# Optimization experiments

Measured on AMD Instinct MI355X. Metric: run time of the kernel, lower is better.

Reference implementation:

```python
import jax, jax.numpy as jnp
import numpy as np

R = 2  # decimation factor


def _cheby1_sos(N=8, rp=0.05, Wn=1.0 / R):
    """Chebyshev type-I lowpass, second-order sections (matches scipy.signal.cheby1 math)."""
    eps = np.sqrt(10.0 ** (rp / 10.0) - 1.0)
    mu = np.arcsinh(1.0 / eps) / N
    k = np.arange(1, N + 1)
    theta = np.pi * (2 * k - 1) / (2 * N)
    # analog prototype poles (no zeros)
    p = -np.sinh(mu) * np.sin(theta) + 1j * np.cosh(mu) * np.cos(theta)
    gain = np.real(np.prod(-p))
    if N % 2 == 0:
        gain /= np.sqrt(1.0 + eps * eps)
    # prewarp + lp2lp
    fs = 2.0
    warped = 2.0 * fs * np.tan(np.pi * Wn / fs)
    p = p * warped
    gain = gain * warped ** N
    # bilinear transform (zeros -> z=-1, order N)
    fs2 = 2.0 * fs
    pz = (fs2 + p) / (fs2 - p)
    gain = gain / np.real(np.prod(fs2 - p))
    # pair complex-conjugate poles into biquads (N even, all complex)
    pp = pz[np.imag(pz) > 0]
    a1 = -2.0 * np.real(pp)
    a2 = np.abs(pp) ** 2
    g = gain ** (1.0 / len(pp))  # distribute gain evenly across sections
    b0 = np.full(len(pp), g)
    sos = np.stack([b0, 2.0 * b0, b0, np.ones(len(pp)), a1, a2], axis=1)
    return sos  # [nsec, 6] float64


_SOS = _cheby1_sos()


def _sosfilt(x):
    """Cascaded biquads, direct form II transposed, zero initial state. x: [B, T]."""
    B = x.shape[0]
    nsec = _SOS.shape[0]
    b0 = jnp.asarray(_SOS[:, 0], x.dtype)
    b1 = jnp.asarray(_SOS[:, 1], x.dtype)
    b2 = jnp.asarray(_SOS[:, 2], x.dtype)
    a1 = jnp.asarray(_SOS[:, 4], x.dtype)
    a2 = jnp.asarray(_SOS[:, 5], x.dtype)

    def step(carry, xt):  # carry: (z1, z2) each [B, nsec]; xt: [B]
        z1, z2 = carry
        y = xt
        nz1, nz2 = [], []
        for s in range(nsec):  # fixed small unroll over sections
            out = b0[s] * y + z1[:, s]
            nz1.append(b1[s] * y + z2[:, s] - a1[s] * out)
            nz2.append(b2[s] * y - a2[s] * out)
            y = out
        return (jnp.stack(nz1, axis=1), jnp.stack(nz2, axis=1)), y

    z0 = jnp.zeros((B, nsec), x.dtype)
    _, ys = jax.lax.scan(step, (z0, z0), x.T)  # scan over time
    return ys.T  # [B, T]


def setup_inputs() -> dict:
    key = jax.random.key(0)
    x = jax.random.normal(key, (32, 131072), dtype=jnp.float32)
    return {"x": x}


def reference(x) -> jnp.ndarray:
    y = _sosfilt(x)
    return y[..., ::R]
```

## Files before the change

### kernel.cpp

```cpp
#include <hip/hip_runtime.h>
#include <cmath>
#include <complex>


#define T_LEN   131072
#define B_ROWS  32
#define L_CHUNK 64
#define H_WARM  192
#define CPR     (T_LEN / L_CHUNK)
#define NTHREADS (B_ROWS * CPR)

struct Coef { float g; float a1[4]; float a2[4]; };

__device__ __forceinline__ float4 ldg4(const float* __restrict__ p, int idx) {
    if (idx >= 0) return *reinterpret_cast<const float4*>(p + idx);
    return make_float4(0.f, 0.f, 0.f, 0.f);
}

__global__ __launch_bounds__(256) void cheby_decimate_kernel(
    const float* __restrict__ x, float* __restrict__ out, Coef c)
{
    const int tid   = blockIdx.x * blockDim.x + threadIdx.x;
    const int row   = tid >> 11;
    const int chunk = tid & (CPR - 1);
    const float* __restrict__ xr = x + (size_t)row * T_LEN;
    float* __restrict__ orow = out + (size_t)row * (T_LEN / 2)
                                   + (size_t)chunk * (L_CHUNK / 2);

    const float g    = c.g;
    const float na10 = -c.a1[0], na20 = -c.a2[0];
    const float na11 = -c.a1[1], na21 = -c.a2[1];
    const float na12 = -c.a1[2], na22 = -c.a2[2];
    const float na13 = -c.a1[3], na23 = -c.a2[3];

    float z11=0.f,z12=0.f, z21=0.f,z22=0.f, z31=0.f,z32=0.f, z41=0.f,z42=0.f;

    const int start = chunk * L_CHUNK - H_WARM;

#define STEP(yv) do {                                                          \
        float y = (yv); float w, o, t;                                         \
        w = g*y; o = w + z11; t = fmaf(2.f, w, z12);                           \
        z11 = fmaf(na10, o, t); z12 = fmaf(na20, o, w); y = o;                 \
        w = g*y; o = w + z21; t = fmaf(2.f, w, z22);                           \
        z21 = fmaf(na11, o, t); z22 = fmaf(na21, o, w); y = o;                 \
        w = g*y; o = w + z31; t = fmaf(2.f, w, z32);                           \
        z31 = fmaf(na12, o, t); z32 = fmaf(na22, o, w); y = o;                 \
        w = g*y; o = w + z41; t = fmaf(2.f, w, z42);                           \
        z41 = fmaf(na13, o, t); z42 = fmaf(na23, o, w); y = o;                 \
        (yv) = y;                                                              \
    } while (0)

    float4 cur = ldg4(xr, start);
    #pragma unroll 4
    for (int gb = 0; gb < H_WARM / 4; ++gb) {
        float4 nxt = ldg4(xr, start + 4 * (gb + 1));
        STEP(cur.x); STEP(cur.y); STEP(cur.z); STEP(cur.w);
        cur = nxt;
    }

    #pragma unroll
    for (int gb = 0; gb < L_CHUNK / 4; ++gb) {
        float4 nxt = make_float4(0.f, 0.f, 0.f, 0.f);
        if (gb + 1 < L_CHUNK / 4)
            nxt = ldg4(xr, start + 4 * (H_WARM / 4 + gb + 1));
        STEP(cur.x); STEP(cur.y); STEP(cur.z); STEP(cur.w);
        reinterpret_cast<float2*>(orow)[gb] = make_float2(cur.x, cur.z);
        cur = nxt;
    }
#undef STEP
}

extern "C" void kernel_launch(void* const* d_in, const int* in_sizes, int n_in,
                              void* d_out, int out_size, void* d_ws, size_t ws_size,
                              hipStream_t stream)
{
    const float* x = (const float*)d_in[0];
    float* out = (float*)d_out;

    const int N = 8;
    const double rp = 0.05;
    const double eps = std::sqrt(std::pow(10.0, rp / 10.0) - 1.0);
    const double mu  = std::asinh(1.0 / eps) / N;

    std::complex<double> p[8];
    std::complex<double> prodnp(1.0, 0.0);
    for (int i = 0; i < N; ++i) {
        double theta = M_PI * (2.0 * (i + 1) - 1.0) / (2.0 * N);
        p[i] = std::complex<double>(-std::sinh(mu) * std::sin(theta),
                                     std::cosh(mu) * std::cos(theta));
        prodnp *= -p[i];
    }
    double gain = prodnp.real() / std::sqrt(1.0 + eps * eps);

    const double fs = 2.0;
    const double warped = 2.0 * fs * std::tan(M_PI * 0.5 / fs);
    std::complex<double> prodden(1.0, 0.0);
    std::complex<double> pz[8];
    for (int i = 0; i < N; ++i) {
        p[i] *= warped;
        pz[i] = (2.0 * fs + p[i]) / (2.0 * fs - p[i]);
        prodden *= (2.0 * fs - p[i]);
    }
    gain *= std::pow(warped, (double)N);
    gain /= prodden.real();

    Coef c;
    int ns = 0;
    double A1[4], A2[4];
    for (int i = 0; i < N; ++i) {
        if (pz[i].imag() > 0.0) {
            A1[ns] = -2.0 * pz[i].real();
            A2[ns] = std::norm(pz[i]);
            ++ns;
        }
    }
    const double gsec = std::pow(gain, 1.0 / ns);
    c.g = (float)gsec;
    for (int s = 0; s < 4; ++s) { c.a1[s] = (float)A1[s]; c.a2[s] = (float)A2[s]; }

    dim3 block(256), grid(NTHREADS / 256);
    hipLaunchKernelGGL(cheby_decimate_kernel, grid, block, 0, stream, x, out, c);
}
```

Measured before the change: 78.46 us.

## Stage input windows and output tiles through swizzled LDS for coalesced access

Each block now loads its contiguous input window plus warmup halo cooperatively into shared memory with coalesced float4 loads, and threads read their chunks from LDS using an XOR swizzle to avoid bank conflicts. Outputs are gathered into registers, transposed through LDS and written back as fully coalesced float4 stores. This removes strided per-thread global loads, redundant halo refetches and uncoalesced float2 stores. In exchange it costs about 66KB of LDS per block, which lowers occupancy, and adds two barriers.

```diff
diff --git a/kernel.cpp b/kernel.cpp
--- a/kernel.cpp
+++ b/kernel.cpp
@@ -5,29 +5,40 @@
 
 #define T_LEN   131072
 #define B_ROWS  32
+#define OUT_LEN (T_LEN / 2)
 #define L_CHUNK 64
 #define H_WARM  192
-#define CPR     (T_LEN / L_CHUNK)
-#define NTHREADS (B_ROWS * CPR)
+#define TPB     256
+#define BLOCKS_PER_ROW (T_LEN / (L_CHUNK * TPB))
+#define WIN_FLOATS (TPB * L_CHUNK + H_WARM)
+#define WIN_UNITS  (WIN_FLOATS / 4)
+#define NBLOCKS (B_ROWS * BLOCKS_PER_ROW)
 
 struct Coef { float g; float a1[4]; float a2[4]; };
-
-__device__ __forceinline__ float4 ldg4(const float* __restrict__ p, int idx) {
-    if (idx >= 0) return *reinterpret_cast<const float4*>(p + idx);
-    return make_float4(0.f, 0.f, 0.f, 0.f);
-}
 
 __global__ __launch_bounds__(256) void cheby_decimate_kernel(
     const float* __restrict__ x, float* __restrict__ out, Coef c)
 {
-    const int tid   = blockIdx.x * blockDim.x + threadIdx.x;
-    const int row   = tid >> 11;
-    const int chunk = tid & (CPR - 1);
+    __shared__ float4 lds[WIN_UNITS];
+    const int t   = threadIdx.x;
+    const int row = blockIdx.x / BLOCKS_PER_ROW;
+    const int bc  = blockIdx.x % BLOCKS_PER_ROW;
     const float* __restrict__ xr = x + (size_t)row * T_LEN;
-    float* __restrict__ orow = out + (size_t)row * (T_LEN / 2)
-                                   + (size_t)chunk * (L_CHUNK / 2);
+    const int wstart = bc * (TPB * L_CHUNK) - H_WARM;
 
-    const float g    = c.g;
+    #pragma unroll
+    for (int k = 0; k < (WIN_UNITS + TPB - 1) / TPB; ++k) {
+        int w = t + TPB * k;
+        if (w < WIN_UNITS) {
+            int g = wstart + 4 * w;
+            float4 v = make_float4(0.f, 0.f, 0.f, 0.f);
+            if (g >= 0) v = *reinterpret_cast<const float4*>(xr + g);
+            lds[w ^ ((w >> 4) & 7)] = v;
+        }
+    }
+    __syncthreads();
+
+    const float g0   = c.g;
     const float na10 = -c.a1[0], na20 = -c.a2[0];
     const float na11 = -c.a1[1], na21 = -c.a2[1];
     const float na12 = -c.a1[2], na22 = -c.a2[2];
@@ -35,39 +46,55 @@
 
     float z11=0.f,z12=0.f, z21=0.f,z22=0.f, z31=0.f,z32=0.f, z41=0.f,z42=0.f;
 
-    const int start = chunk * L_CHUNK - H_WARM;
-
+#define LREAD(u) lds[(u) ^ (((u) >> 4) & 7)]
 #define STEP(yv) do {                                                          \
-        float y = (yv); float w, o, t;                                         \
-        w = g*y; o = w + z11; t = fmaf(2.f, w, z12);                           \
-        z11 = fmaf(na10, o, t); z12 = fmaf(na20, o, w); y = o;                 \
-        w = g*y; o = w + z21; t = fmaf(2.f, w, z22);                           \
-        z21 = fmaf(na11, o, t); z22 = fmaf(na21, o, w); y = o;                 \
-        w = g*y; o = w + z31; t = fmaf(2.f, w, z32);                           \
-        z31 = fmaf(na12, o, t); z32 = fmaf(na22, o, w); y = o;                 \
-        w = g*y; o = w + z41; t = fmaf(2.f, w, z42);                           \
-        z41 = fmaf(na13, o, t); z42 = fmaf(na23, o, w); y = o;                 \
+        float y = (yv); float w_, o, tt;                                       \
+        w_ = g0*y; o = w_ + z11; tt = fmaf(2.f, w_, z12);                      \
+        z11 = fmaf(na10, o, tt); z12 = fmaf(na20, o, w_); y = o;               \
+        w_ = g0*y; o = w_ + z21; tt = fmaf(2.f, w_, z22);                      \
+        z21 = fmaf(na11, o, tt); z22 = fmaf(na21, o, w_); y = o;               \
+        w_ = g0*y; o = w_ + z31; tt = fmaf(2.f, w_, z32);                      \
+        z31 = fmaf(na12, o, tt); z32 = fmaf(na22, o, w_); y = o;               \
+        w_ = g0*y; o = w_ + z41; tt = fmaf(2.f, w_, z42);                      \
+        z41 = fmaf(na13, o, tt); z42 = fmaf(na23, o, w_); y = o;               \
         (yv) = y;                                                              \
     } while (0)
 
-    float4 cur = ldg4(xr, start);
+    const int ub = 16 * t;
+    float4 cur = LREAD(ub);
+    float outv[32];
+
     #pragma unroll 4
-    for (int gb = 0; gb < H_WARM / 4; ++gb) {
-        float4 nxt = ldg4(xr, start + 4 * (gb + 1));
+    for (int j = 0; j < 48; ++j) {
+        float4 nxt = LREAD(ub + j + 1);
         STEP(cur.x); STEP(cur.y); STEP(cur.z); STEP(cur.w);
         cur = nxt;
     }
-
     #pragma unroll
-    for (int gb = 0; gb < L_CHUNK / 4; ++gb) {
-        float4 nxt = make_float4(0.f, 0.f, 0.f, 0.f);
-        if (gb + 1 < L_CHUNK / 4)
-            nxt = ldg4(xr, start + 4 * (H_WARM / 4 + gb + 1));
+    for (int j = 48; j < 64; ++j) {
+        float4 nxt = (j < 63) ? LREAD(ub + j + 1) : make_float4(0.f,0.f,0.f,0.f);
         STEP(cur.x); STEP(cur.y); STEP(cur.z); STEP(cur.w);
-        reinterpret_cast<float2*>(orow)[gb] = make_float2(cur.x, cur.z);
+        outv[2*(j-48)]   = cur.x;
+        outv[2*(j-48)+1] = cur.z;
         cur = nxt;
     }
 #undef STEP
+#undef LREAD
+
+    __syncthreads();
+    #pragma unroll
+    for (int q = 0; q < 8; ++q) {
+        lds[8*t + (q ^ (t & 7))] =
+            make_float4(outv[4*q], outv[4*q+1], outv[4*q+2], outv[4*q+3]);
+    }
+    __syncthreads();
+    const size_t obase = (size_t)row * OUT_LEN + (size_t)bc * (TPB * L_CHUNK / 2);
+    #pragma unroll
+    for (int k = 0; k < 8; ++k) {
+        int v = t + TPB * k;
+        float4 d = lds[(v & ~7) + ((v & 7) ^ ((v >> 3) & 7))];
+        *reinterpret_cast<float4*>(out + obase + 4 * v) = d;
+    }
 }
 
 extern "C" void kernel_launch(void* const* d_in, const int* in_sizes, int n_in,
@@ -118,6 +145,6 @@
     c.g = (float)gsec;
     for (int s = 0; s < 4; ++s) { c.a1[s] = (float)A1[s]; c.a2[s] = (float)A2[s]; }
 
-    dim3 block(256), grid(NTHREADS / 256);
+    dim3 block(TPB), grid(NBLOCKS);
     hipLaunchKernelGGL(cheby_decimate_kernel, grid, block, 0, stream, x, out, c);
 }
```

After: 74.91 us. -4.5%, faster.
